# Kernel optimization log

Hardware: AMD Instinct MI355X
Metric: run time of the kernel (lower is better)

## Reference

```python
import jax, jax.numpy as jnp
import numpy as np

N_THETA, N_GAMMA, HIDDEN = 16, 64, 64
SCENE_DIM, QUERY_DIM = 16, 60
B, N_OBJ = 65536, 10
N_STEPS, DT = 20, 0.01
K_THETA, K_GAMMA, K_CROSS = 1.0, 1.0, 0.5
TWO_PI = 2.0 * np.pi


def setup_inputs() -> dict:
    key = jax.random.key(0)
    ks = jax.random.split(key, 10)
    scene = jax.random.normal(ks[0], (B, N_OBJ, SCENE_DIM), jnp.float32)
    query = jax.random.normal(ks[1], (B, QUERY_DIM), jnp.float32)
    # per-sample seeded initial oscillator state (batched)
    theta_phase0 = jax.random.uniform(ks[2], (B, N_THETA), jnp.float32, 0.0, TWO_PI)
    gamma_phase0 = jax.random.uniform(ks[3], (B, N_GAMMA), jnp.float32, 0.0, TWO_PI)
    theta_freq = TWO_PI * (4.0 + 4.0 * jax.random.uniform(ks[4], (B, N_THETA), jnp.float32))   # theta band 4-8 Hz
    gamma_freq = TWO_PI * (30.0 + 50.0 * jax.random.uniform(ks[5], (B, N_GAMMA), jnp.float32))  # gamma band 30-80 Hz
    init = lambda k, shp, fan: (jax.random.normal(k, shp, jnp.float32) / np.sqrt(fan)).astype(jnp.float32)
    Ws = init(ks[6], (SCENE_DIM, N_GAMMA), SCENE_DIM)
    bs = jnp.zeros((N_GAMMA,), jnp.float32)
    Wq = init(ks[7], (QUERY_DIM, HIDDEN), QUERY_DIM)
    bq = jnp.zeros((HIDDEN,), jnp.float32)
    d_comb = N_THETA + N_GAMMA + HIDDEN  # 144
    W1 = init(ks[8], (d_comb, HIDDEN), d_comb)
    b1 = jnp.zeros((HIDDEN,), jnp.float32)
    W2 = init(ks[9], (HIDDEN, 2), HIDDEN)
    b2 = jnp.zeros((2,), jnp.float32)
    return {"scene": scene, "query": query,
            "theta_phase0": theta_phase0, "theta_freq": theta_freq,
            "gamma_phase0": gamma_phase0, "gamma_freq": gamma_freq,
            "Ws": Ws, "bs": bs, "Wq": Wq, "bq": bq,
            "W1": W1, "b1": b1, "W2": W2, "b2": b2}


def _integrate(theta_phase0, theta_amp0, theta_freq, gamma_phase0, gamma_amp0, gamma_freq):
    """Batched Euler integration of theta-gamma Kuramoto network.

    Mean-field all-to-all coupling: sum_j a_j*sin(p_j - p_i)
      = cos(p_i)*sum_j a_j*sin(p_j) - sin(p_i)*sum_j a_j*cos(p_j).
    """
    def step(carry, _):
        tp, ta, gp, ga = carry  # (B,Nt),(B,Nt),(B,Ng),(B,Ng)
        st, ct = jnp.sin(tp), jnp.cos(tp)
        sg, cg = jnp.sin(gp), jnp.cos(gp)
        # theta intra-population coupling (amplitude-weighted mean field)
        Ti = jnp.sum(ta * st, -1, keepdims=True)
        Tr = jnp.sum(ta * ct, -1, keepdims=True)
        coup_t = (Ti * ct - Tr * st) / N_THETA
        # gamma intra-population coupling
        Gi = jnp.sum(ga * sg, -1, keepdims=True)
        Gr = jnp.sum(ga * cg, -1, keepdims=True)
        coup_g = (Gi * cg - Gr * sg) / N_GAMMA
        # theta -> gamma cross-frequency phase coupling (mean theta field)
        mi = jnp.mean(st, -1, keepdims=True)
        mr = jnp.mean(ct, -1, keepdims=True)
        cross = mi * cg - mr * sg
        dtp = theta_freq + K_THETA * coup_t
        dgp = gamma_freq + K_GAMMA * coup_g + K_CROSS * cross
        dta = ta * (1.0 - ta * ta)   # Stuart-Landau amplitude dynamics
        dga = ga * (1.0 - ga * ga)
        new = (tp + DT * dtp, ta + DT * dta, gp + DT * dgp, ga + DT * dga)
        return new, None

    carry0 = (theta_phase0, theta_amp0, gamma_phase0, gamma_amp0)
    (tp, ta, gp, ga), _ = jax.lax.scan(step, carry0, None, length=N_STEPS)
    return tp, ta, gp, ga


def reference(scene, query, theta_phase0, theta_freq, gamma_phase0, gamma_freq,
              Ws, bs, Wq, bq, W1, b1, W2, b2):
    scene_flat = jnp.mean(scene, axis=1)                      # (B, D_scene)
    gamma_init = jax.nn.sigmoid(scene_flat @ Ws + bs)         # (B, n_gamma)
    gamma_amp0 = jax.lax.stop_gradient(gamma_init)            # .detach() in original
    theta_amp0 = jnp.ones_like(theta_phase0)
    _, ta, _, ga = _integrate(theta_phase0, theta_amp0, theta_freq,
                              gamma_phase0, gamma_amp0, gamma_freq)
    osc_feat = jnp.concatenate([ta, ga], axis=-1)             # (B, n_theta+n_gamma)
    q_feat = query @ Wq + bq                                  # (B, hidden)
    combined = jnp.concatenate([osc_feat, q_feat], axis=-1)   # (B, 144)
    h = jax.nn.relu(combined @ W1 + b1)
    logits = h @ W2 + b2
    return jax.nn.log_softmax(logits, axis=-1)
```

## Files before the change

kernel.cpp:

```cpp
#include <hip/hip_runtime.h>


typedef __fp16 h2_t  __attribute__((ext_vector_type(2)));
typedef __fp16 f16x8 __attribute__((ext_vector_type(8)));
typedef float  f32x4 __attribute__((ext_vector_type(4)));
typedef unsigned u32x4 __attribute__((ext_vector_type(4)));

union H2U { unsigned u; h2_t h; };
union F8  { u32x4 u; f16x8 h; };

__device__ __forceinline__ unsigned pk(float a, float b) {
    H2U v; v.h = __builtin_amdgcn_cvt_pkrtz(a, b);
    return v.u;
}
__device__ __forceinline__ h2_t uh(unsigned x) { H2U v; v.u = x; return v.h; }
__device__ __forceinline__ float dot2(h2_t a, h2_t b, float c) {
    return __builtin_amdgcn_fdot2(a, b, c, false);
}
__device__ __forceinline__ float F20(float g) {
    #pragma unroll
    for (int n = 0; n < 20; ++n) {
        float g2 = g * g;
        g = fmaf(0.01f, g * (1.0f - g2), g);
    }
    return g;
}

#define NW 5826

__global__ void prep_kernel(const float* __restrict__ Ws,
                            const float* __restrict__ bs,
                            const float* __restrict__ Wq,
                            const float* __restrict__ bq,
                            const float* __restrict__ W1,
                            const float* __restrict__ b1,
                            const float* __restrict__ W2,
                            const float* __restrict__ b2,
                            float* __restrict__ ws) {
    unsigned* wsu = (unsigned*)ws;
    int gid = blockIdx.x * 256 + threadIdx.x;
    if (gid < 4096) {
        int j = gid >> 6, p = gid & 63;
        int k0 = 2 * p;
        float va = 0.f, vb = 0.f;
        if (p < 32) {
            va = W1[(16 + k0) * 64 + j];
            vb = W1[(17 + k0) * 64 + j];
        } else if (p < 62) {
            int d0 = k0 - 64;
            float s0 = 0.f, s1 = 0.f;
            #pragma unroll 16
            for (int c = 0; c < 64; ++c) {
                float w = W1[(80 + c) * 64 + j];
                s0 = fmaf(Wq[d0 * 64 + c], w, s0);
                s1 = fmaf(Wq[(d0 + 1) * 64 + c], w, s1);
            }
            va = s0; vb = s1;
        } else if (p == 62) {
            float acc = b1[j];
            #pragma unroll
            for (int r = 0; r < 16; ++r) acc += W1[r * 64 + j];
            #pragma unroll 16
            for (int c = 0; c < 64; ++c)
                acc = fmaf(bq[c], W1[(80 + c) * 64 + j], acc);
            va = acc; vb = 0.f;
        }
        wsu[gid] = pk(va, vb);
    } else if (gid < 4608) {
        int w = gid - 4096, dp = w >> 6, g = w & 63;
        wsu[gid] = pk(0.1f * Ws[(2 * dp) * 64 + g],
                      0.1f * Ws[(2 * dp + 1) * 64 + g]);
    } else if (gid < 5632) {
        int li = gid - 4608, i = li >> 1;
        float x0 = (float)i * 0.015625f - 4.0f;
        float F0 = F20(1.0f / (1.0f + expf(-x0)));
        if (li & 1) {
            float F1 = F20(1.0f / (1.0f + expf(-(x0 + 0.015625f))));
            ws[gid] = F1 - F0;
        } else {
            ws[gid] = F0;
        }
    } else if (gid < 5696) {
        ws[gid] = bs[gid - 5632];
    } else if (gid < 5824) {
        ws[gid] = W2[gid - 5696];
    } else if (gid < 5826) {
        ws[gid] = b2[gid - 5824];
    }
}

#define W0o  0
#define WS2o 4096
#define LUTo 4608
#define BSo  5632
#define W2o  5696
#define SFTo 5824
#define QTo  6336
#define QP   72
#define LDSW (QTo + 32 * QP)

__global__ __launch_bounds__(256, 2) void fused_kernel(
    const float* __restrict__ scene,
    const float* __restrict__ query,
    const float* __restrict__ wsbuf,
    float* __restrict__ out)
{
    __shared__ unsigned lds[LDSW];
    const int t  = threadIdx.x;
    const int eb = blockIdx.x << 6;
    const unsigned* wsu = (const unsigned*)wsbuf;

    #pragma unroll
    for (int i = 0; i < 16; ++i) {
        int widx = t + (i << 8);
        int j7 = (widx >> 6) & 7;
        lds[widx] = wsu[widx ^ (j7 << 2)];
    }
    #pragma unroll
    for (int i = 0; i < 7; ++i) {
        int idx = 4096 + t + (i << 8);
        if (idx < 5824) lds[idx] = wsu[idx];
    }
    {
        const int sel = t >> 2, q4 = t & 3;
        const float4* sp = (const float4*)scene + (size_t)(eb + sel) * 40 + q4;
        float4 a = sp[0];
        #pragma unroll
        for (int o = 1; o < 10; ++o) {
            float4 v = sp[4 * o];
            a.x += v.x; a.y += v.y; a.z += v.z; a.w += v.w;
        }
        lds[SFTo + ((q4 << 1) + 0) * 64 + sel] = pk(a.x, a.y);
        lds[SFTo + ((q4 << 1) + 1) * 64 + sel] = pk(a.z, a.w);
    }
    #pragma unroll
    for (int i = 0; i < 4; ++i) {
        int idx = t + (i << 8);
        if (idx < 960) {
            int qel = idx / 15, kq = idx - qel * 15;
            float4 qv = ((const float4*)query)[(size_t)(eb + qel) * 15 + kq];
            lds[QTo + (2 * kq + 0) * QP + qel] = pk(qv.x, qv.y);
            lds[QTo + (2 * kq + 1) * QP + qel] = pk(qv.z, qv.w);
        }
    }
    if (t < 64)       lds[QTo + 30 * QP + t]        = pk(1.0f, 0.0f);
    else if (t < 128) lds[QTo + 31 * QP + (t - 64)] = 0u;

    __syncthreads();

    const int lane = t & 63;
    const int kb   = lane >> 4;
    const int elb  = ((t >> 6) << 4) | (lane & 15);

    unsigned sf2[8];
    #pragma unroll
    for (int dp = 0; dp < 8; ++dp) sf2[dp] = lds[SFTo + dp * 64 + elb];

    F8 bfrag[4];
    #pragma unroll
    for (int c = 0; c < 2; ++c) {
        float g[8];
        #pragma unroll
        for (int s = 0; s < 2; ++s) {
            unsigned wqa[8][4];
            #pragma unroll
            for (int dp = 0; dp < 8; ++dp) {
                u32x4 w = *(const u32x4*)&lds[WS2o + dp * 64 + (c << 5) + (kb << 3) + (s << 2)];
                wqa[dp][0] = w[0]; wqa[dp][1] = w[1]; wqa[dp][2] = w[2]; wqa[dp][3] = w[3];
            }
            #pragma unroll
            for (int i2 = 0; i2 < 4; ++i2) {
                float x = __uint_as_float(lds[BSo + (c << 5) + (kb << 3) + (s << 2) + i2]);
                #pragma unroll
                for (int dp = 0; dp < 8; ++dp)
                    x = dot2(uh(sf2[dp]), uh(wqa[dp][i2]), x);
                float u = fminf(fmaxf(fmaf(x, 64.0f, 256.0f), 0.0f), 511.0f);
                int   i0 = (int)u;
                float2 e = *(const float2*)&lds[LUTo + (i0 << 1)];
                g[(s << 2) + i2] = fmaf(u - (float)i0, e.y, e.x);
            }
        }
        F8 f;
        f.u[0] = pk(g[0], g[1]); f.u[1] = pk(g[2], g[3]);
        f.u[2] = pk(g[4], g[5]); f.u[3] = pk(g[6], g[7]);
        bfrag[c] = f;
    }
    #pragma unroll
    for (int c2 = 0; c2 < 2; ++c2) {
        F8 f;
        #pragma unroll
        for (int r = 0; r < 4; ++r)
            f.u[r] = lds[QTo + ((kb << 2) + r + (c2 << 4)) * QP + elb];
        bfrag[2 + c2] = f;
    }

    float l0 = 0.f, l1 = 0.f;
    #pragma unroll
    for (int jt = 0; jt < 4; ++jt) {
        f32x4 acc = {0.f, 0.f, 0.f, 0.f};
        const int j = (jt << 4) | (lane & 15);
        #pragma unroll
        for (int c = 0; c < 4; ++c) {
            const int ch = ((c << 2) | kb) ^ (j & 7);
            F8 a;
            a.u = *(const u32x4*)&lds[W0o + (j << 6) + (ch << 2)];
            acc = __builtin_amdgcn_mfma_f32_16x16x32_f16(a.h, bfrag[c].h, acc, 0, 0, 0);
        }
        #pragma unroll
        for (int r = 0; r < 4; ++r) {
            const int jr = (jt << 4) + (kb << 2) + r;
            float hv = fmaxf(acc[r], 0.f);
            float2 wv = *(const float2*)&lds[W2o + (jr << 1)];
            l0 = fmaf(hv, wv.x, l0);
            l1 = fmaf(hv, wv.y, l1);
        }
    }
    l0 += __shfl_xor(l0, 16); l0 += __shfl_xor(l0, 32);
    l1 += __shfl_xor(l1, 16); l1 += __shfl_xor(l1, 32);
    l0 += wsbuf[5824]; l1 += wsbuf[5825];
    if (lane < 16) {
        const float mx = fmaxf(l0, l1);
        const float lz = mx + __logf(__expf(l0 - mx) + __expf(l1 - mx));
        float2 o = { l0 - lz, l1 - lz };
        ((float2*)out)[eb + elb] = o;
    }
}

extern "C" void kernel_launch(void* const* d_in, const int* in_sizes, int n_in,
                              void* d_out, int out_size, void* d_ws, size_t ws_size,
                              hipStream_t stream) {
    const float* scene = (const float*)d_in[0];
    const float* query = (const float*)d_in[1];
    const float* Ws = (const float*)d_in[6];
    const float* bs = (const float*)d_in[7];
    const float* Wq = (const float*)d_in[8];
    const float* bq = (const float*)d_in[9];
    const float* W1 = (const float*)d_in[10];
    const float* b1 = (const float*)d_in[11];
    const float* W2 = (const float*)d_in[12];
    const float* b2 = (const float*)d_in[13];
    float* out = (float*)d_out;
    float* ws  = (float*)d_ws;

    const int B = in_sizes[0] / 160;
    prep_kernel<<<23, 256, 0, stream>>>(Ws, bs, Wq, bq, W1, b1, W2, b2, ws);
    fused_kernel<<<B / 64, 256, 0, stream>>>(scene, query, ws, out);
}
```

Baseline: 27.10 us.

## Process two sample groups per block with prefetch and direct global-to-LDS weight loads

Each block now handles 128 samples in two groups of 64, so the per-block weight staging into shared memory is amortised over twice the work. The second group's scene and query loads are issued into registers before the first group's compute, so their memory latency overlaps with it. Weight staging switches to global_load_lds 16-byte transfers spread across the waves, replacing per-thread load/store loops. The cost is fewer blocks (half the grid), more registers for the prefetched data, and a second activation buffer in LDS, which may reduce occupancy.

```diff
diff --git a/kernel.cpp b/kernel.cpp
--- a/kernel.cpp
+++ b/kernel.cpp
@@ -26,7 +26,7 @@
     return g;
 }
 
-#define NW 5826
+#define NWP 5888
 
 __global__ void prep_kernel(const float* __restrict__ Ws,
                             const float* __restrict__ bs,
@@ -84,8 +84,8 @@
         ws[gid] = bs[gid - 5632];
     } else if (gid < 5824) {
         ws[gid] = W2[gid - 5696];
-    } else if (gid < 5826) {
-        ws[gid] = b2[gid - 5824];
+    } else if (gid < NWP) {
+        ws[gid] = (gid == 5824) ? b2[0] : (gid == 5825) ? b2[1] : 0.f;
     }
 }
 
@@ -94,10 +94,8 @@
 #define LUTo 4608
 #define BSo  5632
 #define W2o  5696
-#define SFTo 5824
-#define QTo  6336
 #define QP   72
-#define LDSW (QTo + 32 * QP)
+#define ACTW 2816
 
 __global__ __launch_bounds__(256, 2) void fused_kernel(
     const float* __restrict__ scene,
@@ -105,24 +103,31 @@
     const float* __restrict__ wsbuf,
     float* __restrict__ out)
 {
-    __shared__ unsigned lds[LDSW];
-    const int t  = threadIdx.x;
-    const int eb = blockIdx.x << 6;
+    __shared__ unsigned lds[NWP];
+    __shared__ unsigned actS[2][ACTW];
+
+    const int t    = threadIdx.x;
+    const int lane = t & 63;
+    const int wv   = __builtin_amdgcn_readfirstlane(t) >> 6;
+    const int eb   = blockIdx.x << 7;
     const unsigned* wsu = (const unsigned*)wsbuf;
 
     #pragma unroll
-    for (int i = 0; i < 16; ++i) {
-        int widx = t + (i << 8);
-        int j7 = (widx >> 6) & 7;
-        lds[widx] = wsu[widx ^ (j7 << 2)];
-    }
-    #pragma unroll
-    for (int i = 0; i < 7; ++i) {
-        int idx = 4096 + t + (i << 8);
-        if (idx < 5824) lds[idx] = wsu[idx];
-    }
+    for (int i = 0; i < 6; ++i) {
+        const int chunk = wv * 6 + i;
+        if (chunk < 23) {
+            const int widx = (chunk << 8) | (lane << 2);
+            const int src  = (widx < 4096) ? (widx ^ (((widx >> 6) & 7) << 2))
+                                           : widx;
+            __builtin_amdgcn_global_load_lds(
+                (const __attribute__((address_space(1))) unsigned*)(wsu + src),
+                (__attribute__((address_space(3))) unsigned*)&lds[chunk << 8],
+                16, 0, 0);
+        }
+    }
+
+    const int sel = t >> 2, q4 = t & 3;
     {
-        const int sel = t >> 2, q4 = t & 3;
         const float4* sp = (const float4*)scene + (size_t)(eb + sel) * 40 + q4;
         float4 a = sp[0];
         #pragma unroll
@@ -130,100 +135,146 @@
             float4 v = sp[4 * o];
             a.x += v.x; a.y += v.y; a.z += v.z; a.w += v.w;
         }
-        lds[SFTo + ((q4 << 1) + 0) * 64 + sel] = pk(a.x, a.y);
-        lds[SFTo + ((q4 << 1) + 1) * 64 + sel] = pk(a.z, a.w);
+        actS[0][((q4 << 1) + 0) * 64 + sel] = pk(a.x, a.y);
+        actS[0][((q4 << 1) + 1) * 64 + sel] = pk(a.z, a.w);
     }
     #pragma unroll
     for (int i = 0; i < 4; ++i) {
-        int idx = t + (i << 8);
+        const int idx = t + (i << 8);
         if (idx < 960) {
-            int qel = idx / 15, kq = idx - qel * 15;
+            const int qel = idx / 15, kq = idx - qel * 15;
             float4 qv = ((const float4*)query)[(size_t)(eb + qel) * 15 + kq];
-            lds[QTo + (2 * kq + 0) * QP + qel] = pk(qv.x, qv.y);
-            lds[QTo + (2 * kq + 1) * QP + qel] = pk(qv.z, qv.w);
-        }
-    }
-    if (t < 64)       lds[QTo + 30 * QP + t]        = pk(1.0f, 0.0f);
-    else if (t < 128) lds[QTo + 31 * QP + (t - 64)] = 0u;
-
+            actS[0][512 + (2 * kq + 0) * QP + qel] = pk(qv.x, qv.y);
+            actS[0][512 + (2 * kq + 1) * QP + qel] = pk(qv.z, qv.w);
+        }
+    }
+    if (t < 64) {
+        actS[0][512 + 30 * QP + t] = pk(1.0f, 0.0f);
+        actS[1][512 + 30 * QP + t] = pk(1.0f, 0.0f);
+    } else if (t < 128) {
+        actS[0][512 + 31 * QP + (t - 64)] = 0u;
+        actS[1][512 + 31 * QP + (t - 64)] = 0u;
+    }
     __syncthreads();
 
-    const int lane = t & 63;
-    const int kb   = lane >> 4;
-    const int elb  = ((t >> 6) << 4) | (lane & 15);
-
-    unsigned sf2[8];
-    #pragma unroll
-    for (int dp = 0; dp < 8; ++dp) sf2[dp] = lds[SFTo + dp * 64 + elb];
-
-    F8 bfrag[4];
-    #pragma unroll
-    for (int c = 0; c < 2; ++c) {
-        float g[8];
-        #pragma unroll
-        for (int s = 0; s < 2; ++s) {
-            unsigned wqa[8][4];
-            #pragma unroll
-            for (int dp = 0; dp < 8; ++dp) {
-                u32x4 w = *(const u32x4*)&lds[WS2o + dp * 64 + (c << 5) + (kb << 3) + (s << 2)];
-                wqa[dp][0] = w[0]; wqa[dp][1] = w[1]; wqa[dp][2] = w[2]; wqa[dp][3] = w[3];
-            }
-            #pragma unroll
-            for (int i2 = 0; i2 < 4; ++i2) {
-                float x = __uint_as_float(lds[BSo + (c << 5) + (kb << 3) + (s << 2) + i2]);
+    float4 sv[10];
+    {
+        const float4* sp1 = (const float4*)scene + (size_t)(eb + 64 + sel) * 40 + q4;
+        #pragma unroll
+        for (int o = 0; o < 10; ++o) sv[o] = sp1[4 * o];
+    }
+    float4 qv1[4];
+    #pragma unroll
+    for (int i = 0; i < 4; ++i) {
+        const int idx = t + (i << 8);
+        if (idx < 960) {
+            const int qel = idx / 15, kq = idx - qel * 15;
+            qv1[i] = ((const float4*)query)[(size_t)(eb + 64 + qel) * 15 + kq];
+        }
+    }
+
+    const int kb  = lane >> 4;
+    const int elb = ((t >> 6) << 4) | (lane & 15);
+
+    auto computeGroup = [&](const unsigned* acts, int ebase) {
+        unsigned sf2[8];
+        #pragma unroll
+        for (int dp = 0; dp < 8; ++dp) sf2[dp] = acts[dp * 64 + elb];
+
+        F8 bfrag[4];
+        #pragma unroll
+        for (int c = 0; c < 2; ++c) {
+            float g[8];
+            #pragma unroll
+            for (int s = 0; s < 2; ++s) {
+                unsigned wqa[8][4];
                 #pragma unroll
-                for (int dp = 0; dp < 8; ++dp)
-                    x = dot2(uh(sf2[dp]), uh(wqa[dp][i2]), x);
-                float u = fminf(fmaxf(fmaf(x, 64.0f, 256.0f), 0.0f), 511.0f);
-                int   i0 = (int)u;
-                float2 e = *(const float2*)&lds[LUTo + (i0 << 1)];
-                g[(s << 2) + i2] = fmaf(u - (float)i0, e.y, e.x);
-            }
-        }
-        F8 f;
-        f.u[0] = pk(g[0], g[1]); f.u[1] = pk(g[2], g[3]);
-        f.u[2] = pk(g[4], g[5]); f.u[3] = pk(g[6], g[7]);
-        bfrag[c] = f;
-    }
-    #pragma unroll
-    for (int c2 = 0; c2 < 2; ++c2) {
-        F8 f;
-        #pragma unroll
-        for (int r = 0; r < 4; ++r)
-            f.u[r] = lds[QTo + ((kb << 2) + r + (c2 << 4)) * QP + elb];
-        bfrag[2 + c2] = f;
-    }
-
-    float l0 = 0.f, l1 = 0.f;
-    #pragma unroll
-    for (int jt = 0; jt < 4; ++jt) {
-        f32x4 acc = {0.f, 0.f, 0.f, 0.f};
-        const int j = (jt << 4) | (lane & 15);
-        #pragma unroll
-        for (int c = 0; c < 4; ++c) {
-            const int ch = ((c << 2) | kb) ^ (j & 7);
-            F8 a;
-            a.u = *(const u32x4*)&lds[W0o + (j << 6) + (ch << 2)];
-            acc = __builtin_amdgcn_mfma_f32_16x16x32_f16(a.h, bfrag[c].h, acc, 0, 0, 0);
-        }
-        #pragma unroll
-        for (int r = 0; r < 4; ++r) {
-            const int jr = (jt << 4) + (kb << 2) + r;
-            float hv = fmaxf(acc[r], 0.f);
-            float2 wv = *(const float2*)&lds[W2o + (jr << 1)];
-            l0 = fmaf(hv, wv.x, l0);
-            l1 = fmaf(hv, wv.y, l1);
-        }
-    }
-    l0 += __shfl_xor(l0, 16); l0 += __shfl_xor(l0, 32);
-    l1 += __shfl_xor(l1, 16); l1 += __shfl_xor(l1, 32);
-    l0 += wsbuf[5824]; l1 += wsbuf[5825];
-    if (lane < 16) {
-        const float mx = fmaxf(l0, l1);
-        const float lz = mx + __logf(__expf(l0 - mx) + __expf(l1 - mx));
-        float2 o = { l0 - lz, l1 - lz };
-        ((float2*)out)[eb + elb] = o;
-    }
+                for (int dp = 0; dp < 8; ++dp) {
+                    u32x4 w = *(const u32x4*)&lds[WS2o + dp * 64 + (c << 5) + (kb << 3) + (s << 2)];
+                    wqa[dp][0] = w[0]; wqa[dp][1] = w[1];
+                    wqa[dp][2] = w[2]; wqa[dp][3] = w[3];
+                }
+                #pragma unroll
+                for (int i2 = 0; i2 < 4; ++i2) {
+                    float x = __uint_as_float(lds[BSo + (c << 5) + (kb << 3) + (s << 2) + i2]);
+                    #pragma unroll
+                    for (int dp = 0; dp < 8; ++dp)
+                        x = dot2(uh(sf2[dp]), uh(wqa[dp][i2]), x);
+                    float u = fminf(fmaxf(fmaf(x, 64.0f, 256.0f), 0.0f), 511.0f);
+                    int   i0 = (int)u;
+                    float2 e = *(const float2*)&lds[LUTo + (i0 << 1)];
+                    g[(s << 2) + i2] = fmaf(u - (float)i0, e.y, e.x);
+                }
+            }
+            F8 f;
+            f.u[0] = pk(g[0], g[1]); f.u[1] = pk(g[2], g[3]);
+            f.u[2] = pk(g[4], g[5]); f.u[3] = pk(g[6], g[7]);
+            bfrag[c] = f;
+        }
+        #pragma unroll
+        for (int c2 = 0; c2 < 2; ++c2) {
+            F8 f;
+            #pragma unroll
+            for (int r = 0; r < 4; ++r)
+                f.u[r] = acts[512 + ((kb << 2) + r + (c2 << 4)) * QP + elb];
+            bfrag[2 + c2] = f;
+        }
+
+        float l0 = 0.f, l1 = 0.f;
+        #pragma unroll
+        for (int jt = 0; jt < 4; ++jt) {
+            f32x4 acc = {0.f, 0.f, 0.f, 0.f};
+            const int j = (jt << 4) | (lane & 15);
+            #pragma unroll
+            for (int c = 0; c < 4; ++c) {
+                const int ch = ((c << 2) | kb) ^ (j & 7);
+                F8 a;
+                a.u = *(const u32x4*)&lds[W0o + (j << 6) + (ch << 2)];
+                acc = __builtin_amdgcn_mfma_f32_16x16x32_f16(a.h, bfrag[c].h, acc, 0, 0, 0);
+            }
+            #pragma unroll
+            for (int r = 0; r < 4; ++r) {
+                const int jr = (jt << 4) + (kb << 2) + r;
+                float hv = fmaxf(acc[r], 0.f);
+                float2 wv2 = *(const float2*)&lds[W2o + (jr << 1)];
+                l0 = fmaf(hv, wv2.x, l0);
+                l1 = fmaf(hv, wv2.y, l1);
+            }
+        }
+        l0 += __shfl_xor(l0, 16); l0 += __shfl_xor(l0, 32);
+        l1 += __shfl_xor(l1, 16); l1 += __shfl_xor(l1, 32);
+        l0 += wsbuf[5824]; l1 += wsbuf[5825];
+        if (lane < 16) {
+            const float mx = fmaxf(l0, l1);
+            const float lz = mx + __logf(__expf(l0 - mx) + __expf(l1 - mx));
+            float2 o = { l0 - lz, l1 - lz };
+            ((float2*)out)[ebase + elb] = o;
+        }
+    };
+
+    computeGroup(actS[0], eb);
+
+    {
+        float4 a = sv[0];
+        #pragma unroll
+        for (int o = 1; o < 10; ++o) {
+            a.x += sv[o].x; a.y += sv[o].y; a.z += sv[o].z; a.w += sv[o].w;
+        }
+        actS[1][((q4 << 1) + 0) * 64 + sel] = pk(a.x, a.y);
+        actS[1][((q4 << 1) + 1) * 64 + sel] = pk(a.z, a.w);
+    }
+    #pragma unroll
+    for (int i = 0; i < 4; ++i) {
+        const int idx = t + (i << 8);
+        if (idx < 960) {
+            const int qel = idx / 15, kq = idx - qel * 15;
+            actS[1][512 + (2 * kq + 0) * QP + qel] = pk(qv1[i].x, qv1[i].y);
+            actS[1][512 + (2 * kq + 1) * QP + qel] = pk(qv1[i].z, qv1[i].w);
+        }
+    }
+    __syncthreads();
+
+    computeGroup(actS[1], eb + 64);
 }
 
 extern "C" void kernel_launch(void* const* d_in, const int* in_sizes, int n_in,
@@ -244,5 +295,5 @@
 
     const int B = in_sizes[0] / 160;
     prep_kernel<<<23, 256, 0, stream>>>(Ws, bs, Wq, bq, W1, b1, W2, b2, ws);
-    fused_kernel<<<B / 64, 256, 0, stream>>>(scene, query, ws, out);
-}
+    fused_kernel<<<B / 128, 256, 0, stream>>>(scene, query, ws, out);
+}
```

Result: faster. 26.01 us (-4.0%).
